# Optimization experiments

Measured on AMD Instinct MI355X. Metric: run time of the kernel, lower is better.

## Reference

```python
import jax, jax.numpy as jnp
import numpy as np

N = 50000   # nodes
E = 150000  # edges
G = 256     # graphs in batch
H0, H1, H2, H3 = 8, 128, 256, 512


def _lin(key, fi, fo):
    return jax.random.normal(key, (fi, fo), dtype=jnp.float32) * (1.0 / np.sqrt(fi))


def setup_inputs() -> dict:
    key = jax.random.key(0)
    ks = jax.random.split(key, 12)
    x = jax.random.normal(ks[0], (N, H0), dtype=jnp.float32)
    edge_index = jax.random.randint(ks[1], (2, E), 0, N)
    edge_weight = jax.random.uniform(ks[2], (E,), dtype=jnp.float32)
    batch = jnp.sort(jax.random.randint(ks[3], (N,), 0, G))
    return {
        'x': x, 'edge_index': edge_index, 'edge_weight': edge_weight, 'batch': batch,
        'W1': _lin(ks[4], H0, H1), 'b1': jnp.zeros((H1,), jnp.float32),
        'W2': _lin(ks[5], H1, H2), 'b2': jnp.zeros((H2,), jnp.float32),
        'W3': _lin(ks[6], H2, H3), 'b3': jnp.zeros((H3,), jnp.float32),
        'Wfc': _lin(ks[7], H3, 1), 'bfc': jnp.zeros((1,), jnp.float32),
    }


def _gcn_conv(h, W, b, src, dst, ew, n):
    # h: [N, Fin] -> [N, Fout]; symmetric GCN normalization (self-loops already in src/dst/ew)
    h = h @ W                                             # [N, Fout]
    deg = jax.ops.segment_sum(ew, dst, num_segments=n)    # [N]
    dinv = jnp.where(deg > 0, jax.lax.rsqrt(deg), 0.0)
    norm = dinv[src] * ew * dinv[dst]                     # [E+N]
    msgs = h[src] * norm[:, None]                         # gather + scale
    out = jax.ops.segment_sum(msgs, dst, num_segments=n)  # scatter-add
    return out + b


def reference(x, edge_index, edge_weight, batch, W1, b1, W2, b2, W3, b3, Wfc, bfc):
    n = x.shape[0]
    loop = jnp.arange(n)
    src = jnp.concatenate([edge_index[0], loop])
    dst = jnp.concatenate([edge_index[1], loop])
    ew = jnp.concatenate([edge_weight, jnp.ones((n,), edge_weight.dtype)])

    h1 = jax.nn.relu(_gcn_conv(x, W1, b1, src, dst, ew, n))
    h2 = jax.nn.relu(_gcn_conv(h1, W2, b2, src, dst, ew, n))
    h3 = jax.nn.relu(_gcn_conv(h2, W3, b3, src, dst, ew, n))

    # global mean pool over graphs
    sums = jax.ops.segment_sum(h3, batch, num_segments=G)              # [G, H3]
    cnt = jax.ops.segment_sum(jnp.ones((n,), h3.dtype), batch, num_segments=G)
    pooled = sums / jnp.maximum(cnt, 1.0)[:, None]

    return jax.nn.sigmoid(pooled @ Wfc + bfc)              # [G, 1]
```

## Files before the change

kernel.cpp:

```cpp
#include <hip/hip_runtime.h>
#include <math.h>

typedef __attribute__((ext_vector_type(8))) short short8;
typedef __attribute__((ext_vector_type(4))) float floatx4;


__device__ __forceinline__ unsigned short f2bf(float f) {
    unsigned int u = __float_as_uint(f);
    unsigned int r = (u + 0x7fffu + ((u >> 16) & 1u)) >> 16;
    return (unsigned short)r;
}
__device__ __forceinline__ float bfu_lo(unsigned int u) {
    return __uint_as_float(u << 16);
}
__device__ __forceinline__ float bfu_hi(unsigned int u) {
    return __uint_as_float(u & 0xffff0000u);
}


__global__ void k_init(float* __restrict__ deg, int* __restrict__ cnt,
                       int* __restrict__ cursor, int N) {
    int i = blockIdx.x * blockDim.x + threadIdx.x;
    if (i < N) { deg[i] = 1.0f; cnt[i] = 0; cursor[i] = 0; }
}

__global__ void k_hist_deg(const int* __restrict__ dst, const float* __restrict__ ew,
                           float* __restrict__ deg, int* __restrict__ cnt, int E) {
    int e = blockIdx.x * blockDim.x + threadIdx.x;
    if (e < E) {
        int d = dst[e];
        atomicAdd(&deg[d], ew[e]);
        atomicAdd(&cnt[d], 1);
    }
}

__global__ __launch_bounds__(256) void k_dinv_scana(float* __restrict__ deg,
                                                    const int* __restrict__ cnt,
                                                    int* __restrict__ bsum, int N) {
    int b = blockIdx.x, t = threadIdx.x;
    int base = b * 1024 + t * 4;
    int s = 0;
#pragma unroll
    for (int j = 0; j < 4; ++j) {
        int i = base + j;
        if (i < N) { deg[i] = rsqrtf(deg[i]); s += cnt[i]; }
    }
    __shared__ int sh[256];
    sh[t] = s; __syncthreads();
    for (int st = 128; st > 0; st >>= 1) { if (t < st) sh[t] += sh[t + st]; __syncthreads(); }
    if (t == 0) bsum[b] = sh[0];
}

__global__ __launch_bounds__(256) void k_scan_b(int* __restrict__ bsum, int nb) {
    int t = threadIdx.x;
    __shared__ int sh[256];
    int orig = (t < nb) ? bsum[t] : 0;
    sh[t] = orig; __syncthreads();
    for (int off = 1; off < 256; off <<= 1) {
        int x = (t >= off) ? sh[t - off] : 0;
        __syncthreads();
        sh[t] += x;
        __syncthreads();
    }
    if (t < nb) bsum[t] = sh[t] - orig;
}

__global__ __launch_bounds__(256) void k_scan_c(const int* __restrict__ cnt,
                                                const int* __restrict__ boff,
                                                int* __restrict__ row_start, int N) {
    int b = blockIdx.x, t = threadIdx.x;
    int base = b * 1024 + t * 4;
    int v[4]; int s = 0;
#pragma unroll
    for (int j = 0; j < 4; ++j) { int i = base + j; v[j] = (i < N) ? cnt[i] : 0; s += v[j]; }
    __shared__ int sh[256];
    sh[t] = s; __syncthreads();
    for (int off = 1; off < 256; off <<= 1) {
        int x = (t >= off) ? sh[t - off] : 0;
        __syncthreads();
        sh[t] += x;
        __syncthreads();
    }
    int excl = sh[t] - s + boff[b];
#pragma unroll
    for (int j = 0; j < 4; ++j) {
        int i = base + j;
        if (i < N) row_start[i] = excl;
        excl += v[j];
        if (i == N - 1) row_start[N] = excl;
    }
}

__global__ void k_scatter_norm(const int* __restrict__ src, const int* __restrict__ dst,
                               const float* __restrict__ ew, const float* __restrict__ dinv,
                               const int* __restrict__ row_start, int* __restrict__ cursor,
                               int* __restrict__ esrc, float* __restrict__ enorm, int E) {
    int e = blockIdx.x * blockDim.x + threadIdx.x;
    if (e >= E) return;
    int d = dst[e], s = src[e];
    int pos = row_start[d] + atomicAdd(&cursor[d], 1);
    esrc[pos] = s;
    enorm[pos] = dinv[s] * ew[e] * dinv[d];
}


__global__ void k_wt_all(const float* __restrict__ W2, unsigned short* __restrict__ WT2,
                         int K2, int F2,
                         const float* __restrict__ W3, unsigned short* __restrict__ WT3,
                         int K3, int F3) {
    int gid = blockIdx.x * blockDim.x + threadIdx.x;
    int n2 = K2 * F2;
    if (gid < n2) {
        int k = gid / F2, n = gid % F2;
        WT2[(size_t)n * K2 + k] = f2bf(W2[gid]);
    } else {
        gid -= n2;
        if (gid >= K3 * F3) return;
        int k = gid / F3, n = gid % F3;
        WT3[(size_t)n * K3 + k] = f2bf(W3[gid]);
    }
}


__global__ __launch_bounds__(256) void k_l1(
    const float* __restrict__ x, const float* __restrict__ dinv,
    const int* __restrict__ esrc, const float* __restrict__ enorm,
    const int* __restrict__ row_start, const float* __restrict__ W1,
    const float* __restrict__ b1, unsigned short* __restrict__ h1, int N) {
    __shared__ float w1s[1024];
    __shared__ float b1s[128];
    int tid = threadIdx.x;
#pragma unroll
    for (int i = tid; i < 1024; i += 256) w1s[i] = W1[i];
    if (tid < 128) b1s[tid] = b1[tid];
    __syncthreads();

    int wave = tid >> 6, lane = tid & 63;
    int n = blockIdx.x * 4 + wave;
    if (n >= N) return;

    float dv = dinv[n];
    float dv2 = dv * dv;
    float a[8];
    float4 v0 = *(const float4*)&x[(size_t)n * 8];
    float4 v1 = *(const float4*)&x[(size_t)n * 8 + 4];
    a[0] = v0.x * dv2; a[1] = v0.y * dv2; a[2] = v0.z * dv2; a[3] = v0.w * dv2;
    a[4] = v1.x * dv2; a[5] = v1.y * dv2; a[6] = v1.z * dv2; a[7] = v1.w * dv2;

    int j0 = row_start[n], j1 = row_start[n + 1];
    for (int j = j0; j < j1; ++j) {
        int s = esrc[j];
        float w = enorm[j];
        float4 u0 = *(const float4*)&x[(size_t)s * 8];
        float4 u1 = *(const float4*)&x[(size_t)s * 8 + 4];
        a[0] += w * u0.x; a[1] += w * u0.y; a[2] += w * u0.z; a[3] += w * u0.w;
        a[4] += w * u1.x; a[5] += w * u1.y; a[6] += w * u1.z; a[7] += w * u1.w;
    }

    float acc0 = b1s[lane], acc1 = b1s[lane + 64];
#pragma unroll
    for (int k = 0; k < 8; ++k) {
        acc0 += a[k] * w1s[k * 128 + lane];
        acc1 += a[k] * w1s[k * 128 + lane + 64];
    }
    h1[(size_t)n * 128 + lane] = f2bf(fmaxf(acc0, 0.f));
    h1[(size_t)n * 128 + lane + 64] = f2bf(fmaxf(acc1, 0.f));
}


__global__ void k_agg_bf(const unsigned short* __restrict__ h, const float* __restrict__ dinv,
                         const int* __restrict__ esrc, const float* __restrict__ enorm,
                         const int* __restrict__ row_start,
                         unsigned short* __restrict__ A,
                         int N, int Mpad, int F, int qsh) {
    int p = blockIdx.x * blockDim.x + threadIdx.x;
    int quart = F >> 2;
    if (p >= Mpad * quart) return;
    int n = p >> qsh;
    int fq = (p & (quart - 1)) << 2;
    size_t oidx = (size_t)n * F + fq;
    if (n >= N) {
        *(ushort4*)&A[oidx] = make_ushort4(0, 0, 0, 0);
        return;
    }
    float dv = dinv[n];
    float dv2 = dv * dv;
    uint2 hv = *(const uint2*)&h[oidx];
    float s0 = bfu_lo(hv.x) * dv2, s1 = bfu_hi(hv.x) * dv2;
    float s2 = bfu_lo(hv.y) * dv2, s3 = bfu_hi(hv.y) * dv2;
    int j0 = row_start[n], j1 = row_start[n + 1];
    for (int j = j0; j < j1; ++j) {
        int s = esrc[j];
        float w = enorm[j];
        uint2 nv = *(const uint2*)&h[(size_t)s * F + fq];
        s0 += w * bfu_lo(nv.x);
        s1 += w * bfu_hi(nv.x);
        s2 += w * bfu_lo(nv.y);
        s3 += w * bfu_hi(nv.y);
    }
    *(ushort4*)&A[oidx] = make_ushort4(f2bf(s0), f2bf(s1), f2bf(s2), f2bf(s3));
}


template <int EPI>
__global__ __launch_bounds__(256, 4) void k_gemm_async(
    const unsigned short* __restrict__ A, const unsigned short* __restrict__ B,
    const float* __restrict__ bias, unsigned short* __restrict__ C,
    const float* __restrict__ Wfc, float* __restrict__ part,
    int M, int Mpad, int K, int Fout, int nbsh) {
    __shared__ __align__(16) unsigned short smem[8192];

    int tid = threadIdx.x, wave = tid >> 6, lane = tid & 63;
    int quad = lane >> 4, r = lane & 15;

    int P = blockIdx.x;
    int r8 = P & 7;
    int q = P >> 3;
    int bnIdx = q & ((1 << nbsh) - 1);
    int g = ((q >> nbsh) << 3) + r8;
    int bm = g * 128, bn = bnIdx * 128;
    int wm = (wave & 1) * 64, wn = (wave >> 1) * 64;

    const unsigned short* gsrc[2] = {A, B};
    const int rb[2] = {bm, bn};

    floatx4 acc[4][4] = {};

    for (int k0 = 0; k0 < K; k0 += 32) {
#pragma unroll
        for (int t = 0; t < 2; ++t) {
#pragma unroll
            for (int i = 0; i < 2; ++i) {
                int qc = wave * 2 + i;
                int idx = qc * 64 + lane;
                int row = idx >> 2, kofs = (idx & 3) << 3;
                const unsigned short* gptr = gsrc[t] + ((size_t)(rb[t] + row) * K + k0 + kofs);
                unsigned short* l = &smem[t * 4096 + qc * 512];
                __builtin_amdgcn_global_load_lds(
                    (const __attribute__((address_space(1))) void*)gptr,
                    (__attribute__((address_space(3))) void*)l, 16, 0, 0);
            }
        }
        __syncthreads();

        short8 ah[4];
#pragma unroll
        for (int mt = 0; mt < 4; ++mt) {
            int m = wm + mt * 16 + r;
            ah[mt] = *(const short8*)&smem[m * 32 + quad * 8];
        }
#pragma unroll
        for (int nt = 0; nt < 4; ++nt) {
            int n = wn + nt * 16 + r;
            short8 bh = *(const short8*)&smem[4096 + n * 32 + quad * 8];
#pragma unroll
            for (int mt = 0; mt < 4; ++mt)
                acc[mt][nt] = __builtin_amdgcn_mfma_f32_16x16x32_bf16(ah[mt], bh, acc[mt][nt], 0, 0, 0);
        }
        __syncthreads();
    }

    float bv[4];
#pragma unroll
    for (int nt = 0; nt < 4; ++nt) bv[nt] = bias[bn + wn + nt * 16 + r];

    if (EPI == 0) {
        float* eps = (float*)&smem[0] + wave * 1024;
#pragma unroll
        for (int mt = 0; mt < 4; ++mt) {
#pragma unroll
            for (int nt = 0; nt < 4; ++nt)
#pragma unroll
                for (int reg = 0; reg < 4; ++reg)
                    eps[(quad * 4 + reg) * 64 + nt * 16 + r] =
                        fmaxf(acc[mt][nt][reg] + bv[nt], 0.f);
#pragma unroll
            for (int i = 0; i < 4; ++i) {
                int fl = i * 64 + lane;
                int ri = fl >> 4, c4 = fl & 15;
                float4 v = *(const float4*)&eps[ri * 64 + c4 * 4];
                int gm = bm + wm + mt * 16 + ri;
                if (gm < M)
                    *(ushort4*)&C[(size_t)gm * Fout + bn + wn + c4 * 4] =
                        make_ushort4(f2bf(v.x), f2bf(v.y), f2bf(v.z), f2bf(v.w));
            }
        }
    } else {
        float* rowsum = (float*)&smem[0];
        if (tid < 128) rowsum[tid] = 0.f;
        __syncthreads();
        float wf[4];
#pragma unroll
        for (int nt = 0; nt < 4; ++nt) wf[nt] = Wfc[bn + wn + nt * 16 + r];
#pragma unroll
        for (int mt = 0; mt < 4; ++mt)
#pragma unroll
            for (int reg = 0; reg < 4; ++reg) {
                float v = 0.f;
#pragma unroll
                for (int nt = 0; nt < 4; ++nt)
                    v += fmaxf(acc[mt][nt][reg] + bv[nt], 0.f) * wf[nt];
                v += __shfl_xor(v, 1);
                v += __shfl_xor(v, 2);
                v += __shfl_xor(v, 4);
                v += __shfl_xor(v, 8);
                if (r == 0) atomicAdd(&rowsum[wm + mt * 16 + quad * 4 + reg], v);
            }
        __syncthreads();
        if (tid < 128) part[(size_t)bnIdx * Mpad + bm + tid] = rowsum[tid];
    }
}


__global__ __launch_bounds__(256) void k_pool2(const float* __restrict__ part,
                                               const int* __restrict__ batch,
                                               const float* __restrict__ bfc,
                                               float* __restrict__ out,
                                               int N, int Mpad, int nchunks, int G) {
    int g = (int)((blockIdx.x * blockDim.x + threadIdx.x) >> 6);
    int lane = threadIdx.x & 63;
    if (g >= G) return;
    int lo = 0, hi = N;
    while (lo < hi) { int m = (lo + hi) >> 1; if (batch[m] < g) lo = m + 1; else hi = m; }
    int start = lo;
    hi = N;
    while (lo < hi) { int m = (lo + hi) >> 1; if (batch[m] < g + 1) lo = m + 1; else hi = m; }
    int end = lo;
    float s = 0.f;
    for (int i = start + lane; i < end; i += 64) {
        float t = 0.f;
        for (int c = 0; c < nchunks; ++c) t += part[(size_t)c * Mpad + i];
        s += t;
    }
#pragma unroll
    for (int off = 32; off > 0; off >>= 1) s += __shfl_down(s, off);
    if (lane == 0) {
        float c = (float)(end - start);
        if (c < 1.f) c = 1.f;
        float z = s / c + bfc[0];
        out[g] = 1.f / (1.f + expf(-z));
    }
}


static inline int cdiv(int a, int b) { return (a + b - 1) / b; }

extern "C" void kernel_launch(void* const* d_in, const int* in_sizes, int n_in,
                              void* d_out, int out_size, void* d_ws, size_t ws_size,
                              hipStream_t stream) {
    const float* x   = (const float*)d_in[0];
    const int*   ei  = (const int*)d_in[1];
    const float* ew  = (const float*)d_in[2];
    const int*   bat = (const int*)d_in[3];
    const float* W1  = (const float*)d_in[4];
    const float* b1  = (const float*)d_in[5];
    const float* W2  = (const float*)d_in[6];
    const float* b2  = (const float*)d_in[7];
    const float* W3  = (const float*)d_in[8];
    const float* b3  = (const float*)d_in[9];
    const float* Wfc = (const float*)d_in[10];
    const float* bfc = (const float*)d_in[11];
    float* out = (float*)d_out;

    const int N  = in_sizes[3];
    const int E  = in_sizes[2];
    const int H1 = in_sizes[5];
    const int H2 = in_sizes[7];
    const int H3 = in_sizes[9];
    const int G  = out_size;
    const int Mpad = cdiv(N, 1024) * 1024;
    const int Npad4 = (N + 4) & ~3;

    const int* srcv = ei;
    const int* dstv = ei + E;

    char* p = (char*)d_ws;
    float* dinv      = (float*)p; p += (size_t)N * 4;
    int*   cnt       = (int*)p;   p += (size_t)N * 4;
    int*   cursor    = (int*)p;   p += (size_t)N * 4;
    int*   bsum      = (int*)p;   p += 256 * 4;
    int*   row_start = (int*)p;   p += (size_t)Npad4 * 4;
    int*   esrc      = (int*)p;   p += (size_t)E * 4;
    float* enorm     = (float*)p; p += (size_t)E * 4;
    float* part      = (float*)p; p += (size_t)(H3 / 128) * Mpad * 4;
    unsigned short* WT2 = (unsigned short*)p; p += (size_t)H1 * H2 * 2;
    unsigned short* WT3 = (unsigned short*)p; p += (size_t)H2 * H3 * 2;
    unsigned short* Abf = (unsigned short*)p; p += (size_t)Mpad * H2 * 2;
    unsigned short* h1  = (unsigned short*)p; p += (size_t)Mpad * H1 * 2;
    unsigned short* h2  = (unsigned short*)p; p += (size_t)Mpad * H2 * 2;

    k_init<<<cdiv(N, 256), 256, 0, stream>>>(dinv, cnt, cursor, N);
    k_hist_deg<<<cdiv(E, 256), 256, 0, stream>>>(dstv, ew, dinv, cnt, E);
    int nb = cdiv(N, 1024);
    k_dinv_scana<<<nb, 256, 0, stream>>>(dinv, cnt, bsum, N);
    k_scan_b<<<1, 256, 0, stream>>>(bsum, nb);
    k_scan_c<<<nb, 256, 0, stream>>>(cnt, bsum, row_start, N);
    k_scatter_norm<<<cdiv(E, 256), 256, 0, stream>>>(srcv, dstv, ew, dinv, row_start,
                                                     cursor, esrc, enorm, E);

    k_wt_all<<<cdiv(H1 * H2 + H2 * H3, 256), 256, 0, stream>>>(W2, WT2, H1, H2, W3, WT3, H2, H3);

    k_l1<<<cdiv(N, 4), 256, 0, stream>>>(x, dinv, esrc, enorm, row_start, W1, b1, h1, N);

    k_agg_bf<<<cdiv(Mpad * (H1 / 4), 256), 256, 0, stream>>>(
        h1, dinv, esrc, enorm, row_start, Abf, N, Mpad, H1, __builtin_ctz(H1) - 2);
    k_gemm_async<0><<<(Mpad / 128) * (H2 / 128), 256, 0, stream>>>(
        Abf, WT2, b2, h2, nullptr, nullptr, N, Mpad, H1, H2, __builtin_ctz(H2 / 128));

    k_agg_bf<<<cdiv(Mpad * (H2 / 4), 256), 256, 0, stream>>>(
        h2, dinv, esrc, enorm, row_start, Abf, N, Mpad, H2, __builtin_ctz(H2) - 2);
    k_gemm_async<1><<<(Mpad / 128) * (H3 / 128), 256, 0, stream>>>(
        Abf, WT3, b3, nullptr, Wfc, part, N, Mpad, H2, H3, __builtin_ctz(H3 / 128));

    k_pool2<<<cdiv(G * 64, 256), 256, 0, stream>>>(part, bat, bfc, out, N, Mpad, H3 / 128, G);
}
```

Baseline: 251.9 us.

## Tile layer-1 as block GEMM and widen aggregation to 8 features per thread

Layer 1 previously had each wave aggregate one node redundantly across all 64 lanes and then do a tiny matvec. It now aggregates 128 nodes per block with one thread per node, stages the results in shared memory and runs an 8x8 register-tiled GEMM against W1 with vectorized bf16 stores. The bf16 aggregation kernel now handles 8 features per thread with 16-byte loads, which halves the number of times edge indices and weights are re-read per node. The costs are fewer threads in the gather phase of layer 1 (only half the block works there) and fewer parallel threads in aggregation, which may hurt latency hiding.

```diff
diff --git a/kernel.cpp b/kernel.cpp
--- a/kernel.cpp
+++ b/kernel.cpp
@@ -122,49 +122,89 @@
 }
 
 
-__global__ __launch_bounds__(256) void k_l1(
+__global__ __launch_bounds__(256) void k_l1_gemm(
     const float* __restrict__ x, const float* __restrict__ dinv,
     const int* __restrict__ esrc, const float* __restrict__ enorm,
     const int* __restrict__ row_start, const float* __restrict__ W1,
     const float* __restrict__ b1, unsigned short* __restrict__ h1, int N) {
-    __shared__ float w1s[1024];
-    __shared__ float b1s[128];
+    __shared__ float As[8][132];
+    __shared__ float Bs[8][128];
+
     int tid = threadIdx.x;
-#pragma unroll
-    for (int i = tid; i < 1024; i += 256) w1s[i] = W1[i];
-    if (tid < 128) b1s[tid] = b1[tid];
+    int bm = blockIdx.x * 128;
+
+#pragma unroll
+    for (int i = tid; i < 1024; i += 256) Bs[i >> 7][i & 127] = W1[i];
+
+    if (tid < 128) {
+        int n = bm + tid;
+        float a[8] = {0, 0, 0, 0, 0, 0, 0, 0};
+        if (n < N) {
+            float dv = dinv[n];
+            float dv2 = dv * dv;
+            float4 v0 = *(const float4*)&x[(size_t)n * 8];
+            float4 v1 = *(const float4*)&x[(size_t)n * 8 + 4];
+            a[0] = v0.x * dv2; a[1] = v0.y * dv2; a[2] = v0.z * dv2; a[3] = v0.w * dv2;
+            a[4] = v1.x * dv2; a[5] = v1.y * dv2; a[6] = v1.z * dv2; a[7] = v1.w * dv2;
+            int j1 = row_start[n + 1];
+            for (int j = row_start[n]; j < j1; ++j) {
+                int s = esrc[j];
+                float w = enorm[j];
+                float4 u0 = *(const float4*)&x[(size_t)s * 8];
+                float4 u1 = *(const float4*)&x[(size_t)s * 8 + 4];
+                a[0] += w * u0.x; a[1] += w * u0.y; a[2] += w * u0.z; a[3] += w * u0.w;
+                a[4] += w * u1.x; a[5] += w * u1.y; a[6] += w * u1.z; a[7] += w * u1.w;
+            }
+        }
+#pragma unroll
+        for (int k = 0; k < 8; ++k) As[k][tid] = a[k];
+    }
     __syncthreads();
 
-    int wave = tid >> 6, lane = tid & 63;
-    int n = blockIdx.x * 4 + wave;
-    if (n >= N) return;
-
-    float dv = dinv[n];
-    float dv2 = dv * dv;
-    float a[8];
-    float4 v0 = *(const float4*)&x[(size_t)n * 8];
-    float4 v1 = *(const float4*)&x[(size_t)n * 8 + 4];
-    a[0] = v0.x * dv2; a[1] = v0.y * dv2; a[2] = v0.z * dv2; a[3] = v0.w * dv2;
-    a[4] = v1.x * dv2; a[5] = v1.y * dv2; a[6] = v1.z * dv2; a[7] = v1.w * dv2;
-
-    int j0 = row_start[n], j1 = row_start[n + 1];
-    for (int j = j0; j < j1; ++j) {
-        int s = esrc[j];
-        float w = enorm[j];
-        float4 u0 = *(const float4*)&x[(size_t)s * 8];
-        float4 u1 = *(const float4*)&x[(size_t)s * 8 + 4];
-        a[0] += w * u0.x; a[1] += w * u0.y; a[2] += w * u0.z; a[3] += w * u0.w;
-        a[4] += w * u1.x; a[5] += w * u1.y; a[6] += w * u1.z; a[7] += w * u1.w;
-    }
-
-    float acc0 = b1s[lane], acc1 = b1s[lane + 64];
+    int tx = tid & 15;
+    int ty = tid >> 4;
+    float acc[8][8];
+#pragma unroll
+    for (int i = 0; i < 8; ++i)
+#pragma unroll
+        for (int j = 0; j < 8; ++j) acc[i][j] = 0.f;
+
 #pragma unroll
     for (int k = 0; k < 8; ++k) {
-        acc0 += a[k] * w1s[k * 128 + lane];
-        acc1 += a[k] * w1s[k * 128 + lane + 64];
-    }
-    h1[(size_t)n * 128 + lane] = f2bf(fmaxf(acc0, 0.f));
-    h1[(size_t)n * 128 + lane + 64] = f2bf(fmaxf(acc1, 0.f));
+        float a[8], b[8];
+        float4 a0 = *(const float4*)&As[k][ty * 4];
+        float4 a1 = *(const float4*)&As[k][ty * 4 + 64];
+        float4 b0 = *(const float4*)&Bs[k][tx * 4];
+        float4 b1 = *(const float4*)&Bs[k][tx * 4 + 64];
+        a[0] = a0.x; a[1] = a0.y; a[2] = a0.z; a[3] = a0.w;
+        a[4] = a1.x; a[5] = a1.y; a[6] = a1.z; a[7] = a1.w;
+        b[0] = b0.x; b[1] = b0.y; b[2] = b0.z; b[3] = b0.w;
+        b[4] = b1.x; b[5] = b1.y; b[6] = b1.z; b[7] = b1.w;
+#pragma unroll
+        for (int i = 0; i < 8; ++i)
+#pragma unroll
+            for (int j = 0; j < 8; ++j) acc[i][j] += a[i] * b[j];
+    }
+
+    float4 bi0 = *(const float4*)&b1[tx * 4];
+    float4 bi1 = *(const float4*)&b1[tx * 4 + 64];
+    float bb[8] = {bi0.x, bi0.y, bi0.z, bi0.w, bi1.x, bi1.y, bi1.z, bi1.w};
+#pragma unroll
+    for (int i = 0; i < 8; ++i) {
+        int gm = bm + ((i < 4) ? (ty * 4 + i) : (64 + ty * 4 + i - 4));
+        if (gm >= N) continue;
+        ushort4 v0, v1;
+        v0.x = f2bf(fmaxf(acc[i][0] + bb[0], 0.f));
+        v0.y = f2bf(fmaxf(acc[i][1] + bb[1], 0.f));
+        v0.z = f2bf(fmaxf(acc[i][2] + bb[2], 0.f));
+        v0.w = f2bf(fmaxf(acc[i][3] + bb[3], 0.f));
+        v1.x = f2bf(fmaxf(acc[i][4] + bb[4], 0.f));
+        v1.y = f2bf(fmaxf(acc[i][5] + bb[5], 0.f));
+        v1.z = f2bf(fmaxf(acc[i][6] + bb[6], 0.f));
+        v1.w = f2bf(fmaxf(acc[i][7] + bb[7], 0.f));
+        *(ushort4*)&h1[(size_t)gm * 128 + tx * 4] = v0;
+        *(ushort4*)&h1[(size_t)gm * 128 + tx * 4 + 64] = v1;
+    }
 }
 
 
@@ -172,33 +212,40 @@
                          const int* __restrict__ esrc, const float* __restrict__ enorm,
                          const int* __restrict__ row_start,
                          unsigned short* __restrict__ A,
-                         int N, int Mpad, int F, int qsh) {
+                         int N, int Mpad, int F, int osh) {
     int p = blockIdx.x * blockDim.x + threadIdx.x;
-    int quart = F >> 2;
-    if (p >= Mpad * quart) return;
-    int n = p >> qsh;
-    int fq = (p & (quart - 1)) << 2;
-    size_t oidx = (size_t)n * F + fq;
+    int oct = F >> 3;
+    if (p >= Mpad * oct) return;
+    int n = p >> osh;
+    int fo = (p & (oct - 1)) << 3;
+    size_t oidx = (size_t)n * F + fo;
     if (n >= N) {
-        *(ushort4*)&A[oidx] = make_ushort4(0, 0, 0, 0);
+        *(uint4*)&A[oidx] = make_uint4(0, 0, 0, 0);
         return;
     }
     float dv = dinv[n];
     float dv2 = dv * dv;
-    uint2 hv = *(const uint2*)&h[oidx];
+    uint4 hv = *(const uint4*)&h[oidx];
     float s0 = bfu_lo(hv.x) * dv2, s1 = bfu_hi(hv.x) * dv2;
     float s2 = bfu_lo(hv.y) * dv2, s3 = bfu_hi(hv.y) * dv2;
-    int j0 = row_start[n], j1 = row_start[n + 1];
-    for (int j = j0; j < j1; ++j) {
+    float s4 = bfu_lo(hv.z) * dv2, s5 = bfu_hi(hv.z) * dv2;
+    float s6 = bfu_lo(hv.w) * dv2, s7 = bfu_hi(hv.w) * dv2;
+    int j1 = row_start[n + 1];
+    for (int j = row_start[n]; j < j1; ++j) {
         int s = esrc[j];
         float w = enorm[j];
-        uint2 nv = *(const uint2*)&h[(size_t)s * F + fq];
-        s0 += w * bfu_lo(nv.x);
-        s1 += w * bfu_hi(nv.x);
-        s2 += w * bfu_lo(nv.y);
-        s3 += w * bfu_hi(nv.y);
-    }
-    *(ushort4*)&A[oidx] = make_ushort4(f2bf(s0), f2bf(s1), f2bf(s2), f2bf(s3));
+        uint4 nv = *(const uint4*)&h[(size_t)s * F + fo];
+        s0 += w * bfu_lo(nv.x); s1 += w * bfu_hi(nv.x);
+        s2 += w * bfu_lo(nv.y); s3 += w * bfu_hi(nv.y);
+        s4 += w * bfu_lo(nv.z); s5 += w * bfu_hi(nv.z);
+        s6 += w * bfu_lo(nv.w); s7 += w * bfu_hi(nv.w);
+    }
+    uint4 o;
+    o.x = (unsigned int)f2bf(s0) | ((unsigned int)f2bf(s1) << 16);
+    o.y = (unsigned int)f2bf(s2) | ((unsigned int)f2bf(s3) << 16);
+    o.z = (unsigned int)f2bf(s4) | ((unsigned int)f2bf(s5) << 16);
+    o.w = (unsigned int)f2bf(s6) | ((unsigned int)f2bf(s7) << 16);
+    *(uint4*)&A[oidx] = o;
 }
 
 
@@ -400,15 +447,15 @@
 
     k_wt_all<<<cdiv(H1 * H2 + H2 * H3, 256), 256, 0, stream>>>(W2, WT2, H1, H2, W3, WT3, H2, H3);
 
-    k_l1<<<cdiv(N, 4), 256, 0, stream>>>(x, dinv, esrc, enorm, row_start, W1, b1, h1, N);
-
-    k_agg_bf<<<cdiv(Mpad * (H1 / 4), 256), 256, 0, stream>>>(
-        h1, dinv, esrc, enorm, row_start, Abf, N, Mpad, H1, __builtin_ctz(H1) - 2);
+    k_l1_gemm<<<cdiv(N, 128), 256, 0, stream>>>(x, dinv, esrc, enorm, row_start, W1, b1, h1, N);
+
+    k_agg_bf<<<cdiv(Mpad * (H1 / 8), 256), 256, 0, stream>>>(
+        h1, dinv, esrc, enorm, row_start, Abf, N, Mpad, H1, __builtin_ctz(H1) - 3);
     k_gemm_async<0><<<(Mpad / 128) * (H2 / 128), 256, 0, stream>>>(
         Abf, WT2, b2, h2, nullptr, nullptr, N, Mpad, H1, H2, __builtin_ctz(H2 / 128));
 
-    k_agg_bf<<<cdiv(Mpad * (H2 / 4), 256), 256, 0, stream>>>(
-        h2, dinv, esrc, enorm, row_start, Abf, N, Mpad, H2, __builtin_ctz(H2) - 2);
+    k_agg_bf<<<cdiv(Mpad * (H2 / 8), 256), 256, 0, stream>>>(
+        h2, dinv, esrc, enorm, row_start, Abf, N, Mpad, H2, __builtin_ctz(H2) - 3);
     k_gemm_async<1><<<(Mpad / 128) * (H3 / 128), 256, 0, stream>>>(
         Abf, WT3, b3, nullptr, Wfc, part, N, Mpad, H2, H3, __builtin_ctz(H3 / 128));
 
```

Result: faster. 226.4 us (-10.1%).
